# Kernel tuning notes

Measured on AMD Instinct MI355X. Metric: run time of the kernel, lower is better.

## Reference

```python
import jax, jax.numpy as jnp
import numpy as np

B, N, D, H, P = 4, 512, 256, 8, 3
HD = D // H
EPS = 1e-5

def _ln(x, g, b):
    m = jnp.mean(x, axis=-1, keepdims=True)
    v = jnp.var(x, axis=-1, keepdims=True)
    return (x - m) * jax.lax.rsqrt(v + EPS) * g + b

def setup_inputs() -> dict:
    key = jax.random.key(0)
    ks = jax.random.split(key, 12)
    s = lambda *sh: 1.0 / np.sqrt(sh[0])
    return {
        "x": jax.random.normal(ks[0], (B, N, D), jnp.float32),
        "mask": jax.random.randint(ks[1], (B, N), 0, 2).astype(bool),
        "pair_feat": jax.random.normal(ks[2], (B, N, N, P), jnp.float32),
        "Wqkv": jax.random.normal(ks[3], (D, 3 * D), jnp.float32) * s(D),
        "Wout": jax.random.normal(ks[4], (D, D), jnp.float32) * s(D),
        "bout": jnp.zeros((D,), jnp.float32),
        "Wp1": jax.random.normal(ks[5], (P, D), jnp.float32) * s(P),
        "bp1": jnp.zeros((D,), jnp.float32),
        "Wp2": jax.random.normal(ks[6], (D, H), jnp.float32) * s(D),
        "bp2": jnp.zeros((H,), jnp.float32),
        "Wf1": jax.random.normal(ks[7], (D, 4 * D), jnp.float32) * s(D),
        "bf1": jnp.zeros((4 * D,), jnp.float32),
        "Wf2": jax.random.normal(ks[8], (4 * D, D), jnp.float32) * s(4 * D),
        "bf2": jnp.zeros((D,), jnp.float32),
        "g1": jnp.ones((D,), jnp.float32), "b1": jnp.zeros((D,), jnp.float32),
        "g2": jnp.ones((D,), jnp.float32), "b2": jnp.zeros((D,), jnp.float32),
    }

def reference(x, mask, pair_feat, Wqkv, Wout, bout, Wp1, bp1, Wp2, bp2,
              Wf1, bf1, Wf2, bf2, g1, b1, g2, b2):
    b_, n_, d_ = x.shape
    scale = HD ** -0.5
    qkv = x @ Wqkv                                  # [B,N,3D]
    q, k, v = jnp.split(qkv, 3, axis=-1)
    q = q.reshape(b_, n_, H, HD)
    k = k.reshape(b_, n_, H, HD)
    v = v.reshape(b_, n_, H, HD)
    logits = jnp.einsum('bihd,bjhd->bhij', q, k) * scale
    # pairwise bias MLP -> per-head bias [B,H,N,N]
    bias = jax.nn.relu(pair_feat @ Wp1 + bp1) @ Wp2 + bp2   # [B,N,N,H]
    logits = logits + jnp.transpose(bias, (0, 3, 1, 2))
    key_mask = ~mask[:, None, None, :]               # [B,1,1,N]
    logits = jnp.where(key_mask, -1e9, logits)
    attn = jax.nn.softmax(logits, axis=-1)
    out = jnp.einsum('bhij,bjhd->bihd', attn, v).reshape(b_, n_, d_)
    out = out @ Wout + bout
    x = _ln(x + out, g1, b1)
    h = jax.nn.gelu(x @ Wf1 + bf1, approximate=False) @ Wf2 + bf2
    return _ln(x + h, g2, b2)
```

## Files before the change

### kernel.cpp

```cpp
#include <hip/hip_runtime.h>
#include <hip/hip_fp16.h>
#include <math.h>

typedef unsigned short u16;
typedef short s16x8 __attribute__((ext_vector_type(8)));
typedef _Float16 f16x8 __attribute__((ext_vector_type(8)));
typedef float f32x4 __attribute__((ext_vector_type(4)));
typedef unsigned int u32x2 __attribute__((ext_vector_type(2)));

constexpr int CB = 4, CN = 512, CD = 256, CH = 8, CHD = 32;
constexpr float CEPS = 1e-5f;
constexpr int M_ROWS = CB * CN;
constexpr float QSCALE = 0.17677669529663687f;

constexpr size_t O_XB    = 0;
constexpr size_t O_QB    = 1048576;
constexpr size_t O_KB    = 2097152;
constexpr size_t O_VT    = 3145728;
constexpr size_t O_WQKVT = 4194304;
constexpr size_t O_WOUTT = O_WQKVT + 393216;
constexpr size_t O_WF1T  = O_WOUTT + 131072;
constexpr size_t O_WF2T  = O_WF1T + 524288;
constexpr size_t O_WP2T  = O_WF2T + 524288;
constexpr size_t O_PACKED= O_WP2T + 8192;
constexpr size_t O_JIDX  = O_PACKED + 4096;
constexpr size_t O_BIAS  = O_JIDX + 8192;
constexpr size_t O_AOUT  = O_BIAS + 16777216;
constexpr size_t O_H1B   = O_AOUT + 1048576;
constexpr size_t O_PRE1  = O_H1B + 4194304;
constexpr size_t O_PRE2  = O_PRE1 + 2097152;
constexpr size_t O_CNT   = O_PRE2 + 2097152;
constexpr size_t O_IPOS  = O_CNT + 256;

__device__ inline u16 f2b(float f) {
  union { float f; unsigned u; } v{f};
  return (u16)((v.u + 0x7FFFu + ((v.u >> 16) & 1u)) >> 16);
}
__device__ inline float b2f(u16 b) {
  union { unsigned u; float f; } v{(unsigned)b << 16};
  return v.f;
}
__device__ inline f32x4 MFMA(s16x8 a, s16x8 b, f32x4 c) {
  return __builtin_amdgcn_mfma_f32_16x16x32_bf16(a, b, c, 0, 0, 0);
}
__device__ inline f32x4 MFMAH(f16x8 a, f16x8 b, f32x4 c) {
  return __builtin_amdgcn_mfma_f32_16x16x32_f16(a, b, c, 0, 0, 0);
}
__device__ inline unsigned cvtpk(float lo, float hi) {
  unsigned r;
  asm("v_cvt_pk_bf16_f32 %0, %1, %2" : "=v"(r) : "v"(lo), "v"(hi));
  return r;
}
__device__ inline unsigned pkmax0(unsigned a) {
  unsigned d;
  asm("v_pk_max_f16 %0, %1, 0" : "=v"(d) : "v"(a));
  return d;
}

__global__ __launch_bounds__(256) void prep_kernel(
    const float* __restrict__ x, const float* __restrict__ Wqkv,
    const float* __restrict__ Wp2,
    const float* __restrict__ Wp1, const float* __restrict__ bp1,
    const unsigned char* __restrict__ maskraw,
    u16* __restrict__ xb, u16* __restrict__ wqkvt, u16* __restrict__ wp2t,
    unsigned* __restrict__ packed, int* __restrict__ jidxg,
    int* __restrict__ cntg, int* __restrict__ iposg) {
  __shared__ int mode_max;
  __shared__ int mdec[2048];
  int blk = blockIdx.x, tid = threadIdx.x;
  if (blk < 256) {
    for (int t = tid; t < 512; t += 256) {
      float4 v = ((const float4*)x)[blk * 512 + t];
      u16 o0 = f2b(v.x), o1 = f2b(v.y), o2 = f2b(v.z), o3 = f2b(v.w);
      u32x2 w; w.x = (unsigned)o0 | ((unsigned)o1 << 16);
      w.y = (unsigned)o2 | ((unsigned)o3 << 16);
      *(u32x2*)(xb + (size_t)(blk * 512 + t) * 4) = w;
    }
  } else if (blk < 352) {
    int o0 = (blk - 256) * 2048;
    for (int t = tid; t < 2048; t += 256) {
      int o = o0 + t, n = o >> 8, k = o & 255;
      wqkvt[o] = f2b(Wqkv[k * 768 + n]);
    }
  } else if (blk == 352) {
    for (int t = tid; t < 4096; t += 256) {
      int h = t >> 8, c = t & 255;
      wp2t[t] = (h < 8) ? __half_as_ushort(__float2half(Wp2[c * 8 + h])) : (u16)0;
    }
    if (tid < 128) {
      int p = tid * 2;
      unsigned w0 = (unsigned)__half_as_ushort(__float2half(Wp1[p]))
                  | ((unsigned)__half_as_ushort(__float2half(Wp1[p + 1])) << 16);
      unsigned w1 = (unsigned)__half_as_ushort(__float2half(Wp1[256 + p]))
                  | ((unsigned)__half_as_ushort(__float2half(Wp1[256 + p + 1])) << 16);
      unsigned w2 = (unsigned)__half_as_ushort(__float2half(Wp1[512 + p]))
                  | ((unsigned)__half_as_ushort(__float2half(Wp1[512 + p + 1])) << 16);
      unsigned bb = (unsigned)__half_as_ushort(__float2half(bp1[p]))
                  | ((unsigned)__half_as_ushort(__float2half(bp1[p + 1])) << 16);
      uint4 o; o.x = w0; o.y = w1; o.z = w2; o.w = bb;
      ((uint4*)packed)[tid] = o;
    }
  } else {
    if (tid == 0) mode_max = 0;
    __syncthreads();
    int lm = 0;
    for (int i = tid; i < CB*CN; i += 256)
      if ((i & 3) != 0) lm = max(lm, (int)maskraw[i]);
    atomicMax(&mode_max, lm);
    __syncthreads();
    int mv = mode_max;
    for (int i = tid; i < CB*CN; i += 256) {
      int val;
      if (mv == 0)      val = (((const int*)maskraw)[i] != 0);
      else if (mv == 1) val = (maskraw[i] != 0);
      else              val = (((const unsigned int*)maskraw)[i] != 0);
      mdec[i] = val;
    }
    __syncthreads();
    int w = tid >> 6, lane = tid & 63;
    if (w < 4) {
      int b = w, basei = 0, basem = 0;
      for (int c = 0; c < 8; ++c) {
        int j = c * 64 + lane;
        int m = mdec[b * 512 + j];
        unsigned long long bal = __ballot(m != 0);
        int off  = __popcll(bal & ((1ull << lane) - 1ull));
        int offm = __popcll(~bal & ((1ull << lane) - 1ull));
        int pos;
        if (m) { pos = basei + off; jidxg[b * 512 + pos] = j; }
        else   { pos = 511 - (basem + offm); }
        iposg[b * 512 + j] = pos;
        basei += (int)__popcll(bal);
        basem += (int)(64 - __popcll(bal));
      }
      if (lane == 0) cntg[b] = basei;
      for (int p = basei + lane; p < 512; p += 64) jidxg[b * 512 + p] = 0;
    }
  }
}

__global__ __launch_bounds__(256) void qkv_pbias_kernel(
    const u16* __restrict__ A, const u16* __restrict__ Wt,
    u16* __restrict__ qb, u16* __restrict__ kb, u16* __restrict__ vt,
    const float* __restrict__ pf, const unsigned* __restrict__ packed,
    const u16* __restrict__ wp2t, const float* __restrict__ bp2,
    const int* __restrict__ jidxg, const int* __restrict__ cntg,
    const int* __restrict__ iposg, u16* __restrict__ biasc,
    const float* __restrict__ Wout, const float* __restrict__ Wf1,
    const float* __restrict__ Wf2, u16* __restrict__ woutt,
    u16* __restrict__ wf1t, u16* __restrict__ wf2t) {
  __shared__ uint4 smem[1024];
  const int blk = blockIdx.x, tid = threadIdx.x;
  const int lane = tid & 63, w = tid >> 6;
  if (blk < 384) {
    u16* As = (u16*)smem;
    u16* Bs = (u16*)smem + 64 * 64;
    const int wm = w >> 1, wn = w & 1;
    const int bm = (blk / 12) * 64, bn = (blk % 12) * 64;
    f32x4 fz = {0.f, 0.f, 0.f, 0.f};
    f32x4 acc[2][2] = {{fz, fz}, {fz, fz}};
    for (int k0 = 0; k0 < 256; k0 += 64) {
#pragma unroll
      for (int t = tid; t < 512; t += 256) {
        int r = t >> 3, s = t & 7;
        s16x8 v = *(const s16x8*)(A + (size_t)(bm + r) * 256 + k0 + s * 8);
        *(s16x8*)(As + r * 64 + ((s ^ (r & 7)) << 3)) = v;
      }
#pragma unroll
      for (int t = tid; t < 512; t += 256) {
        int r = t >> 3, s = t & 7;
        s16x8 v = *(const s16x8*)(Wt + (size_t)(bn + r) * 256 + k0 + s * 8);
        *(s16x8*)(Bs + r * 64 + ((s ^ (r & 7)) << 3)) = v;
      }
      __syncthreads();
#pragma unroll
      for (int ks = 0; ks < 2; ++ks) {
        s16x8 af[2], bf[2];
#pragma unroll
        for (int mf = 0; mf < 2; ++mf) {
          int r = wm * 32 + mf * 16 + (lane & 15);
          int s = ks * 4 + (lane >> 4);
          af[mf] = *(const s16x8*)(As + r * 64 + ((s ^ (r & 7)) << 3));
        }
#pragma unroll
        for (int nf = 0; nf < 2; ++nf) {
          int r = wn * 32 + nf * 16 + (lane & 15);
          int s = ks * 4 + (lane >> 4);
          bf[nf] = *(const s16x8*)(Bs + r * 64 + ((s ^ (r & 7)) << 3));
        }
#pragma unroll
        for (int mf = 0; mf < 2; ++mf)
#pragma unroll
          for (int nf = 0; nf < 2; ++nf)
            acc[mf][nf] = MFMA(af[mf], bf[nf], acc[mf][nf]);
      }
      __syncthreads();
    }
#pragma unroll
    for (int mf = 0; mf < 2; ++mf) {
#pragma unroll
      for (int nf = 0; nf < 2; ++nf) {
#pragma unroll
        for (int r = 0; r < 4; ++r) {
          int m = bm + wm * 32 + mf * 16 + (lane >> 4) * 4 + r;
          int n = bn + wn * 32 + nf * 16 + (lane & 15);
          float v = acc[mf][nf][r];
          if (n < 256) {
            qb[(size_t)m * 256 + n] = f2b(v * QSCALE);
          } else if (n < 512) {
            kb[(size_t)m * 256 + (n - 256)] = f2b(v);
          } else {
            int nv = n - 512, h = nv >> 5, d = nv & 31;
            int bb = m >> 9, j = m & 511;
            int pos = iposg[bb * 512 + j];
            vt[(size_t)((bb * 8 + h) * 32 + d) * 512 + pos] = f2b(v);
          }
        }
      }
    }
  } else if (blk < 2432) {
    uint4* pk = smem;
    float* pfl = (float*)(smem + 128);
    int* ji = (int*)(smem + 512);
    const int bid = blk - 384;
    const int b = bid >> 9, i = bid & 511;
    const int q = lane >> 4, hr = lane & 15;
    if (tid < 128) pk[tid] = ((const uint4*)packed)[tid];
    const float4* pfr = (const float4*)(pf + (size_t)(b * 512 + i) * 1536);
#pragma unroll
    for (int t = tid; t < 384; t += 256) ((float4*)pfl)[t] = pfr[t];
    for (int t = tid; t < 512; t += 256) ji[t] = jidxg[b * 512 + t];
    const int cnt = cntg[b];
    __syncthreads();
    __half2 f0d[8], f1d[8], f2d[8];
#pragma unroll
    for (int t = 0; t < 8; ++t) {
      int g = t * 4 + w;
      if (g * 16 < cnt) {
        int jsrc = ji[g * 16 + hr];
        f0d[t] = __float2half2_rn(pfl[jsrc * 3 + 0]);
        f1d[t] = __float2half2_rn(pfl[jsrc * 3 + 1]);
        f2d[t] = __float2half2_rn(pfl[jsrc * 3 + 2]);
      }
    }
    f32x4 fz = {0.f, 0.f, 0.f, 0.f};
    f32x4 acc[8] = {fz, fz, fz, fz, fz, fz, fz, fz};
    for (int chunk = 0; chunk < 8; ++chunk) {
      f16x8 wfrag = *(const f16x8*)(wp2t + hr * 256 + chunk * 32 + q * 8);
      int pbase = chunk * 16 + q * 4;
      __half2 w0[4], w1[4], w2[4], bb[4];
#pragma unroll
      for (int p = 0; p < 4; ++p) {
        uint4 c = pk[pbase + p];
        w0[p] = *(const __half2*)&c.x;
        w1[p] = *(const __half2*)&c.y;
        w2[p] = *(const __half2*)&c.z;
        bb[p] = *(const __half2*)&c.w;
      }
#pragma unroll
      for (int t = 0; t < 8; ++t) {
        int g = t * 4 + w;
        if (g * 16 < cnt) {
          union { unsigned u[4]; f16x8 v; } af;
#pragma unroll
          for (int p = 0; p < 4; ++p) {
            __half2 h = __hfma2(f0d[t], w0[p], bb[p]);
            h = __hfma2(f1d[t], w1[p], h);
            h = __hfma2(f2d[t], w2[p], h);
            af.u[p] = pkmax0(*(const unsigned*)&h);
          }
          acc[t] = MFMAH(af.v, wfrag, acc[t]);
        }
      }
    }
    if (hr < 8) {
      float bb = bp2[hr];
      size_t base = ((size_t)(b * 8 + hr) * 512 + i) * 512;
#pragma unroll
      for (int t = 0; t < 8; ++t) {
        int g = t * 4 + w;
        if (g * 16 < cnt) {
          int p0 = g * 16 + q * 4;
          u32x2 o;
          o.x = cvtpk(acc[t][0] + bb, acc[t][1] + bb);
          o.y = cvtpk(acc[t][2] + bb, acc[t][3] + bb);
          *(u32x2*)(biasc + base + p0) = o;
        }
      }
    }
  } else if (blk < 2464) {
    int o0 = (blk - 2432) * 2048;
    for (int t = tid; t < 2048; t += 256) {
      int o = o0 + t, n = o >> 8, k = o & 255;
      woutt[o] = f2b(Wout[k * 256 + n]);
    }
  } else if (blk < 2592) {
    int o0 = (blk - 2464) * 2048;
    for (int t = tid; t < 2048; t += 256) {
      int o = o0 + t, n = o >> 8, k = o & 255;
      wf1t[o] = f2b(Wf1[k * 1024 + n]);
    }
  } else {
    int o0 = (blk - 2592) * 2048;
    for (int t = tid; t < 2048; t += 256) {
      int o = o0 + t, n = o >> 10, k = o & 1023;
      wf2t[o] = f2b(Wf2[k * 256 + n]);
    }
  }
}

__global__ __launch_bounds__(512) void flash_kernel(
    const u16* __restrict__ qb, const u16* __restrict__ kb,
    const u16* __restrict__ vt, const u16* __restrict__ biasc,
    const int* __restrict__ jidxg, const int* __restrict__ cntg,
    u16* __restrict__ aout) {
  const int i0 = blockIdx.x * 64, h = blockIdx.y, b = blockIdx.z;
  const int tid = threadIdx.x;
  const int lane = tid & 63, w = tid >> 6;
  const int mf = w & 3, jhalf = w >> 2;
  __shared__ u16 qs[64 * 32];
  __shared__ u16 ksh[128 * 32];
  __shared__ u16 vs[32 * 128];
  __shared__ u16 ps[8][16 * 64];
  __shared__ float cmb[4][2][16][2];
  __shared__ int ji[512];
  for (int t = tid; t < 512; t += 512) ji[t] = jidxg[b * 512 + t];
  for (int t = tid; t < 256; t += 512) {
    int r = t >> 2, s = t & 3;
    s16x8 v = *(const s16x8*)(qb + (size_t)(b * 512 + i0 + r) * 256 + h * 32 + s * 8);
    *(s16x8*)(qs + r * 32 + ((s ^ (r & 3)) << 3)) = v;
  }
  const int cnt = cntg[b];
  __syncthreads();
  f32x4 fz = {0.f, 0.f, 0.f, 0.f};
  f32x4 oacc[2] = {fz, fz};
  float mrun[4] = {-3e38f, -3e38f, -3e38f, -3e38f};
  float lrun[4] = {0.f, 0.f, 0.f, 0.f};
  const int jj0 = jhalf * 64;
  const int il = mf * 16 + (lane >> 4) * 4;
  const u16* bbase = biasc + ((size_t)((b * 8 + h) * 512 + i0 + il)) * 512
                   + jj0 + (lane & 15);
  const int NJT = (cnt + 127) >> 7;
  for (int jc = 0; jc < NJT; ++jc) {
    int j0 = jc * 128;
    {
      int r = tid >> 2, s = tid & 3;
      int jsrc = ji[j0 + r];
      s16x8 v = *(const s16x8*)(kb + (size_t)(b * 512 + jsrc) * 256 + h * 32 + s * 8);
      *(s16x8*)(ksh + r * 32 + ((s ^ (r & 3)) << 3)) = v;
    }
    {
      int r = tid >> 4, s = tid & 15;
      s16x8 v = *(const s16x8*)(vt + (size_t)((b * 8 + h) * 32 + r) * 512 + j0 + s * 8);
      *(s16x8*)(vs + r * 128 + (((s & 8) | ((s & 7) ^ (r & 7))) << 3)) = v;
    }
    u16 bvr[4][4];
#pragma unroll
    for (int jf = 0; jf < 4; ++jf)
#pragma unroll
      for (int r = 0; r < 4; ++r)
        bvr[jf][r] = bbase[(size_t)r * 512 + j0 + jf * 16];
    __syncthreads();
    int mk[4];
#pragma unroll
    for (int jf = 0; jf < 4; ++jf)
      mk[jf] = (j0 + jj0 + jf * 16 + (lane & 15)) < cnt;
    int arow = mf * 16 + (lane & 15);
    s16x8 af = *(const s16x8*)(qs + arow * 32 + (((lane >> 4) ^ (arow & 3)) << 3));
    f32x4 sm[4];
#pragma unroll
    for (int jf = 0; jf < 4; ++jf) {
      int brow = jj0 + jf * 16 + (lane & 15);
      s16x8 bfr = *(const s16x8*)(ksh + brow * 32 + (((lane >> 4) ^ (brow & 3)) << 3));
      sm[jf] = MFMA(af, bfr, fz);
    }
#pragma unroll
    for (int jf = 0; jf < 4; ++jf) {
#pragma unroll
      for (int r = 0; r < 4; ++r) {
        float sval = sm[jf][r] + b2f(bvr[jf][r]);
        sm[jf][r] = mk[jf] ? sval : -1e9f;
      }
    }
    float mx[4];
#pragma unroll
    for (int r = 0; r < 4; ++r)
      mx[r] = fmaxf(fmaxf(sm[0][r], sm[1][r]), fmaxf(sm[2][r], sm[3][r]));
#pragma unroll
    for (int d = 1; d < 16; d <<= 1)
#pragma unroll
      for (int r = 0; r < 4; ++r) mx[r] = fmaxf(mx[r], __shfl_xor(mx[r], d));
    float psl[4] = {0.f, 0.f, 0.f, 0.f};
#pragma unroll
    for (int jf = 0; jf < 4; ++jf)
#pragma unroll
      for (int r = 0; r < 4; ++r) {
        float p = __expf(sm[jf][r] - mx[r]);
        sm[jf][r] = p; psl[r] += p;
      }
#pragma unroll
    for (int d = 1; d < 16; d <<= 1)
#pragma unroll
      for (int r = 0; r < 4; ++r) psl[r] += __shfl_xor(psl[r], d);
    if ((lane & 15) == 0) {
#pragma unroll
      for (int r = 0; r < 4; ++r) {
        int row = (lane >> 4) * 4 + r;
        cmb[mf][jhalf][row][0] = mx[r];
        cmb[mf][jhalf][row][1] = psl[r];
      }
    }
    __syncthreads();
    float selfs[4];
#pragma unroll
    for (int r = 0; r < 4; ++r) {
      int row = (lane >> 4) * 4 + r;
      float omx = cmb[mf][1 - jhalf][row][0];
      float ops = cmb[mf][1 - jhalf][row][1];
      float tm = fmaxf(mx[r], omx);
      float nm = fmaxf(mrun[r], tm);
      float sc = __expf(mrun[r] - nm);
      selfs[r] = __expf(mx[r] - nm);
      float ptile = psl[r] * selfs[r] + ops * __expf(omx - nm);
      lrun[r] = lrun[r] * sc + ptile;
      mrun[r] = nm;
      oacc[0][r] *= sc; oacc[1][r] *= sc;
    }
    u16* pw = &ps[w][0];
#pragma unroll
    for (int jf = 0; jf < 4; ++jf) {
      int jcol = jf * 16 + (lane & 15);
      int slot = jcol >> 3, el = jcol & 7;
#pragma unroll
      for (int r = 0; r < 4; ++r) {
        int row = (lane >> 4) * 4 + r;
        pw[row * 64 + ((slot ^ (row & 7)) << 3) + el] = f2b(sm[jf][r] * selfs[r]);
      }
    }
#pragma unroll
    for (int kw = 0; kw < 2; ++kw) {
      int prow = lane & 15;
      s16x8 pa = *(const s16x8*)(pw + prow * 64 + (((kw * 4 + (lane >> 4)) ^ (prow & 7)) << 3));
#pragma unroll
      for (int df = 0; df < 2; ++df) {
        int drow = df * 16 + (lane & 15);
        int jcol = jj0 + kw * 32 + ((lane >> 4) << 3);
        int slot = jcol >> 3;
        s16x8 vv = *(const s16x8*)(vs + drow * 128 + (((slot & 8) | ((slot & 7) ^ (drow & 7))) << 3));
        oacc[df] = MFMA(pa, vv, oacc[df]);
      }
    }
    __syncthreads();
  }
  float* obuf = (float*)&ps[0][0];
  if (jhalf == 1) {
#pragma unroll
    for (int r = 0; r < 4; ++r) {
      int row = mf * 16 + (lane >> 4) * 4 + r;
#pragma unroll
      for (int df = 0; df < 2; ++df)
        obuf[row * 33 + df * 16 + (lane & 15)] = oacc[df][r];
    }
  }
  __syncthreads();
  if (jhalf == 0) {
#pragma unroll
    for (int r = 0; r < 4; ++r) {
      float inv = 1.0f / lrun[r];
      int row = mf * 16 + (lane >> 4) * 4 + r;
      int i = i0 + row;
#pragma unroll
      for (int df = 0; df < 2; ++df) {
        int d = df * 16 + (lane & 15);
        float o = (oacc[df][r] + obuf[row * 33 + d]) * inv;
        aout[(size_t)(b * 512 + i) * 256 + h * 32 + d] = f2b(o);
      }
    }
  }
}

__global__ __launch_bounds__(256) void mgemm_res(
    const u16* __restrict__ A, const u16* __restrict__ Wt,
    const float* __restrict__ bias, const float* __restrict__ R,
    float* __restrict__ outf, int N, int K) {
  __shared__ u16 As[32 * 64];
  __shared__ u16 Bs[64 * 64];
  const int tid = threadIdx.x;
  const int lane = tid & 63, w = tid >> 6;
  const int wm = w >> 1, wn = w & 1;
  const int bm = blockIdx.y * 32, bn = blockIdx.x * 64;
  f32x4 fz = {0.f, 0.f, 0.f, 0.f};
  f32x4 acc[2] = {fz, fz};
  for (int k0 = 0; k0 < K; k0 += 64) {
    for (int t = tid; t < 256; t += 256) {
      int r = t >> 3, s = t & 7;
      s16x8 v = *(const s16x8*)(A + (size_t)(bm + r) * K + k0 + s * 8);
      *(s16x8*)(As + r * 64 + ((s ^ (r & 7)) << 3)) = v;
    }
#pragma unroll
    for (int t = tid; t < 512; t += 256) {
      int r = t >> 3, s = t & 7;
      s16x8 v = *(const s16x8*)(Wt + (size_t)(bn + r) * K + k0 + s * 8);
      *(s16x8*)(Bs + r * 64 + ((s ^ (r & 7)) << 3)) = v;
    }
    __syncthreads();
#pragma unroll
    for (int ks = 0; ks < 2; ++ks) {
      int r = wm * 16 + (lane & 15);
      int s = ks * 4 + (lane >> 4);
      s16x8 af = *(const s16x8*)(As + r * 64 + ((s ^ (r & 7)) << 3));
#pragma unroll
      for (int nf = 0; nf < 2; ++nf) {
        int br = wn * 32 + nf * 16 + (lane & 15);
        s16x8 bf = *(const s16x8*)(Bs + br * 64 + ((s ^ (br & 7)) << 3));
        acc[nf] = MFMA(af, bf, acc[nf]);
      }
    }
    __syncthreads();
  }
#pragma unroll
  for (int nf = 0; nf < 2; ++nf) {
#pragma unroll
    for (int r = 0; r < 4; ++r) {
      int m = bm + wm * 16 + (lane >> 4) * 4 + r;
      int n = bn + wn * 32 + nf * 16 + (lane & 15);
      outf[(size_t)m * N + n] = acc[nf][r] + bias[n] + R[(size_t)m * N + n];
    }
  }
}

__global__ __launch_bounds__(256) void ffn1_kernel(
    const float* __restrict__ pre1, const u16* __restrict__ Wt,
    const float* __restrict__ bias, const float* __restrict__ g1,
    const float* __restrict__ b1, u16* __restrict__ outb) {
  __shared__ u16 As[64 * 64];
  __shared__ u16 Bs[64 * 64];
  __shared__ float rowm[64], rowr[64];
  const int tid = threadIdx.x;
  const int lane = tid & 63, w = tid >> 6;
  const int wm = w >> 1, wn = w & 1;
  const int bm = blockIdx.y * 64, bn = blockIdx.x * 64;
  {
    int r = tid >> 2, qd = tid & 3;
    const float4* pr = (const float4*)(pre1 + (size_t)(bm + r) * 256 + qd * 64);
    float s = 0.f, ss = 0.f;
#pragma unroll
    for (int u = 0; u < 16; ++u) {
      float4 v = pr[u];
      s += v.x + v.y + v.z + v.w;
      ss += v.x*v.x + v.y*v.y + v.z*v.z + v.w*v.w;
    }
    s += __shfl_xor(s, 1); ss += __shfl_xor(ss, 1);
    s += __shfl_xor(s, 2); ss += __shfl_xor(ss, 2);
    if (qd == 0) {
      float mean = s * (1.0f / 256.0f);
      float var  = ss * (1.0f / 256.0f) - mean * mean;
      rowm[r] = mean; rowr[r] = rsqrtf(var + CEPS);
    }
  }
  __syncthreads();
  f32x4 fz = {0.f, 0.f, 0.f, 0.f};
  f32x4 acc[2][2] = {{fz, fz}, {fz, fz}};
  for (int k0 = 0; k0 < 256; k0 += 64) {
#pragma unroll
    for (int t = tid; t < 512; t += 256) {
      int r = t >> 3, s = t & 7;
      float mean = rowm[r], rstd = rowr[r];
      const float4* pr = (const float4*)(pre1 + (size_t)(bm + r) * 256 + k0 + s * 8);
      float4 a0 = pr[0], a1 = pr[1];
      const float4* gp = (const float4*)(g1 + k0 + s * 8);
      const float4* bp = (const float4*)(b1 + k0 + s * 8);
      float4 g0 = gp[0], g1v = gp[1], c0 = bp[0], c1 = bp[1];
      union { unsigned u[4]; s16x8 v; } pk2;
      pk2.u[0] = cvtpk((a0.x-mean)*rstd*g0.x + c0.x, (a0.y-mean)*rstd*g0.y + c0.y);
      pk2.u[1] = cvtpk((a0.z-mean)*rstd*g0.z + c0.z, (a0.w-mean)*rstd*g0.w + c0.w);
      pk2.u[2] = cvtpk((a1.x-mean)*rstd*g1v.x + c1.x, (a1.y-mean)*rstd*g1v.y + c1.y);
      pk2.u[3] = cvtpk((a1.z-mean)*rstd*g1v.z + c1.z, (a1.w-mean)*rstd*g1v.w + c1.w);
      *(s16x8*)(As + r * 64 + ((s ^ (r & 7)) << 3)) = pk2.v;
    }
#pragma unroll
    for (int t = tid; t < 512; t += 256) {
      int r = t >> 3, s = t & 7;
      s16x8 v = *(const s16x8*)(Wt + (size_t)(bn + r) * 256 + k0 + s * 8);
      *(s16x8*)(Bs + r * 64 + ((s ^ (r & 7)) << 3)) = v;
    }
    __syncthreads();
#pragma unroll
    for (int ks = 0; ks < 2; ++ks) {
      s16x8 af[2], bf[2];
#pragma unroll
      for (int mf = 0; mf < 2; ++mf) {
        int r = wm * 32 + mf * 16 + (lane & 15);
        int s = ks * 4 + (lane >> 4);
        af[mf] = *(const s16x8*)(As + r * 64 + ((s ^ (r & 7)) << 3));
      }
#pragma unroll
      for (int nf = 0; nf < 2; ++nf) {
        int r = wn * 32 + nf * 16 + (lane & 15);
        int s = ks * 4 + (lane >> 4);
        bf[nf] = *(const s16x8*)(Bs + r * 64 + ((s ^ (r & 7)) << 3));
      }
#pragma unroll
      for (int mf = 0; mf < 2; ++mf)
#pragma unroll
        for (int nf = 0; nf < 2; ++nf)
          acc[mf][nf] = MFMA(af[mf], bf[nf], acc[mf][nf]);
    }
    __syncthreads();
  }
#pragma unroll
  for (int mf = 0; mf < 2; ++mf) {
#pragma unroll
    for (int nf = 0; nf < 2; ++nf) {
#pragma unroll
      for (int r = 0; r < 4; ++r) {
        int m = bm + wm * 32 + mf * 16 + (lane >> 4) * 4 + r;
        int n = bn + wn * 32 + nf * 16 + (lane & 15);
        float gv = acc[mf][nf][r] + bias[n];
        gv = 0.5f * gv * (1.0f + erff(gv * 0.70710678118654752f));
        outb[(size_t)m * 1024 + n] = f2b(gv);
      }
    }
  }
}

__global__ __launch_bounds__(256) void ffn2_kernel(
    const u16* __restrict__ A, const u16* __restrict__ Wt,
    const float* __restrict__ bias, const float* __restrict__ pre1,
    const float* __restrict__ g1, const float* __restrict__ b1,
    float* __restrict__ outf) {
  __shared__ u16 As[32 * 64];
  __shared__ u16 Bs[64 * 64];
  __shared__ float rowm[32], rowr[32];
  const int tid = threadIdx.x;
  const int lane = tid & 63, w = tid >> 6;
  const int wm = w >> 1, wn = w & 1;
  const int bm = blockIdx.y * 32, bn = blockIdx.x * 64;
  {
    int r = tid >> 3, od = tid & 7;
    const float4* pr = (const float4*)(pre1 + (size_t)(bm + r) * 256 + od * 32);
    float s = 0.f, ss = 0.f;
#pragma unroll
    for (int u = 0; u < 8; ++u) {
      float4 v = pr[u];
      s += v.x + v.y + v.z + v.w;
      ss += v.x*v.x + v.y*v.y + v.z*v.z + v.w*v.w;
    }
    s += __shfl_xor(s, 1); ss += __shfl_xor(ss, 1);
    s += __shfl_xor(s, 2); ss += __shfl_xor(ss, 2);
    s += __shfl_xor(s, 4); ss += __shfl_xor(ss, 4);
    if (od == 0) {
      float mean = s * (1.0f / 256.0f);
      float var  = ss * (1.0f / 256.0f) - mean * mean;
      rowm[r] = mean; rowr[r] = rsqrtf(var + CEPS);
    }
  }
  __syncthreads();
  f32x4 fz = {0.f, 0.f, 0.f, 0.f};
  f32x4 acc[2] = {fz, fz};
  for (int k0 = 0; k0 < 1024; k0 += 64) {
    for (int t = tid; t < 256; t += 256) {
      int r = t >> 3, s = t & 7;
      s16x8 v = *(const s16x8*)(A + (size_t)(bm + r) * 1024 + k0 + s * 8);
      *(s16x8*)(As + r * 64 + ((s ^ (r & 7)) << 3)) = v;
    }
#pragma unroll
    for (int t = tid; t < 512; t += 256) {
      int r = t >> 3, s = t & 7;
      s16x8 v = *(const s16x8*)(Wt + (size_t)(bn + r) * 1024 + k0 + s * 8);
      *(s16x8*)(Bs + r * 64 + ((s ^ (r & 7)) << 3)) = v;
    }
    __syncthreads();
#pragma unroll
    for (int ks = 0; ks < 2; ++ks) {
      int r = wm * 16 + (lane & 15);
      int s = ks * 4 + (lane >> 4);
      s16x8 af = *(const s16x8*)(As + r * 64 + ((s ^ (r & 7)) << 3));
#pragma unroll
      for (int nf = 0; nf < 2; ++nf) {
        int br = wn * 32 + nf * 16 + (lane & 15);
        s16x8 bf = *(const s16x8*)(Bs + br * 64 + ((s ^ (br & 7)) << 3));
        acc[nf] = MFMA(af, bf, acc[nf]);
      }
    }
    __syncthreads();
  }
#pragma unroll
  for (int nf = 0; nf < 2; ++nf) {
#pragma unroll
    for (int r = 0; r < 4; ++r) {
      int m = bm + wm * 16 + (lane >> 4) * 4 + r;
      int n = bn + wn * 32 + nf * 16 + (lane & 15);
      float mean = rowm[m - bm], rstd = rowr[m - bm];
      float xr = (pre1[(size_t)m * 256 + n] - mean) * rstd * g1[n] + b1[n];
      outf[(size_t)m * 256 + n] = acc[nf][r] + bias[n] + xr;
    }
  }
}

__global__ __launch_bounds__(256) void ln_kernel(
    const float* __restrict__ in, const float* __restrict__ g,
    const float* __restrict__ be, float* __restrict__ op) {
  int row = blockIdx.x * 4 + (threadIdx.x >> 6);
  int lane = threadIdx.x & 63;
  const float* x = in + (size_t)row * CD;
  float4 v = *(const float4*)&x[lane * 4];
  float s  = v.x + v.y + v.z + v.w;
  float ss = v.x*v.x + v.y*v.y + v.z*v.z + v.w*v.w;
#pragma unroll
  for (int off = 32; off > 0; off >>= 1) {
    s  += __shfl_xor(s, off);
    ss += __shfl_xor(ss, off);
  }
  float mean = s * (1.0f / CD);
  float var  = ss * (1.0f / CD) - mean * mean;
  float inv  = rsqrtf(var + CEPS);
  float4 gg = *(const float4*)&g[lane * 4];
  float4 bb = *(const float4*)&be[lane * 4];
  float4 o;
  o.x = (v.x - mean) * inv * gg.x + bb.x;
  o.y = (v.y - mean) * inv * gg.y + bb.y;
  o.z = (v.z - mean) * inv * gg.z + bb.z;
  o.w = (v.w - mean) * inv * gg.w + bb.w;
  *(float4*)&op[(size_t)row * CD + lane * 4] = o;
}

extern "C" void kernel_launch(void* const* d_in, const int* in_sizes, int n_in,
                              void* d_out, int out_size, void* d_ws, size_t ws_size,
                              hipStream_t stream) {
  (void)in_sizes; (void)n_in; (void)out_size; (void)ws_size;
  const float* x    = (const float*)d_in[0];
  const void*  mask = d_in[1];
  const float* pf   = (const float*)d_in[2];
  const float* Wqkv = (const float*)d_in[3];
  const float* Wout = (const float*)d_in[4];
  const float* bout = (const float*)d_in[5];
  const float* Wp1  = (const float*)d_in[6];
  const float* bp1  = (const float*)d_in[7];
  const float* Wp2  = (const float*)d_in[8];
  const float* bp2  = (const float*)d_in[9];
  const float* Wf1  = (const float*)d_in[10];
  const float* bf1  = (const float*)d_in[11];
  const float* Wf2  = (const float*)d_in[12];
  const float* bf2  = (const float*)d_in[13];
  const float* g1   = (const float*)d_in[14];
  const float* b1   = (const float*)d_in[15];
  const float* g2   = (const float*)d_in[16];
  const float* b2   = (const float*)d_in[17];

  char* ws = (char*)d_ws;
  u16* xb     = (u16*)(ws + O_XB);
  u16* qb     = (u16*)(ws + O_QB);
  u16* kb     = (u16*)(ws + O_KB);
  u16* vt     = (u16*)(ws + O_VT);
  u16* wqkvt  = (u16*)(ws + O_WQKVT);
  u16* woutt  = (u16*)(ws + O_WOUTT);
  u16* wf1t   = (u16*)(ws + O_WF1T);
  u16* wf2t   = (u16*)(ws + O_WF2T);
  u16* wp2t   = (u16*)(ws + O_WP2T);
  unsigned* packed = (unsigned*)(ws + O_PACKED);
  int* jidxg  = (int*)(ws + O_JIDX);
  int* cntg   = (int*)(ws + O_CNT);
  int* iposg  = (int*)(ws + O_IPOS);
  u16* biasc  = (u16*)(ws + O_BIAS);
  u16* aout   = (u16*)(ws + O_AOUT);
  u16* h1b    = (u16*)(ws + O_H1B);
  float* pre1 = (float*)(ws + O_PRE1);
  float* pre2 = (float*)(ws + O_PRE2);
  float* out  = (float*)d_out;

  hipLaunchKernelGGL(prep_kernel, dim3(354), dim3(256), 0, stream,
                     x, Wqkv, Wp2, Wp1, bp1,
                     (const unsigned char*)mask,
                     xb, wqkvt, wp2t, packed, jidxg, cntg, iposg);
  hipLaunchKernelGGL(qkv_pbias_kernel, dim3(2720), dim3(256), 0, stream,
                     xb, wqkvt, qb, kb, vt,
                     pf, packed, wp2t, bp2, jidxg, cntg, iposg, biasc,
                     Wout, Wf1, Wf2, woutt, wf1t, wf2t);
  hipLaunchKernelGGL(flash_kernel, dim3(8, 8, 4), dim3(512), 0, stream,
                     qb, kb, vt, biasc, jidxg, cntg, aout);
  hipLaunchKernelGGL(mgemm_res, dim3(4, 64), dim3(256), 0, stream,
                     aout, woutt, bout, x, pre1, 256, 256);
  hipLaunchKernelGGL(ffn1_kernel, dim3(16, 32), dim3(256), 0, stream,
                     pre1, wf1t, bf1, g1, b1, h1b);
  hipLaunchKernelGGL(ffn2_kernel, dim3(4, 64), dim3(256), 0, stream,
                     h1b, wf2t, bf2, pre1, g1, b1, pre2);
  hipLaunchKernelGGL(ln_kernel, dim3(M_ROWS / 4), dim3(256), 0, stream,
                     pre2, g2, b2, out);
}
```

Before: 95.37 us.

## Fuse layernorms into full-row output GEMM epilogues and drop standalone LN kernel

```diff
diff --git a/kernel.cpp b/kernel.cpp
--- a/kernel.cpp
+++ b/kernel.cpp
@@ -27,9 +27,9 @@
 constexpr size_t O_BIAS  = O_JIDX + 8192;
 constexpr size_t O_AOUT  = O_BIAS + 16777216;
 constexpr size_t O_H1B   = O_AOUT + 1048576;
-constexpr size_t O_PRE1  = O_H1B + 4194304;
-constexpr size_t O_PRE2  = O_PRE1 + 2097152;
-constexpr size_t O_CNT   = O_PRE2 + 2097152;
+constexpr size_t O_X1B   = O_H1B + 4194304;
+constexpr size_t O_XRF   = O_X1B + 1048576;
+constexpr size_t O_CNT   = O_XRF + 2097152;
 constexpr size_t O_IPOS  = O_CNT + 256;
 
 __device__ inline u16 f2b(float f) {
@@ -479,104 +479,113 @@
   }
 }
 
-__global__ __launch_bounds__(256) void mgemm_res(
+__global__ __launch_bounds__(256) void gemm_ln1_kernel(
     const u16* __restrict__ A, const u16* __restrict__ Wt,
-    const float* __restrict__ bias, const float* __restrict__ R,
-    float* __restrict__ outf, int N, int K) {
-  __shared__ u16 As[32 * 64];
+    const float* __restrict__ bias, const float* __restrict__ x,
+    const float* __restrict__ g1, const float* __restrict__ b1,
+    u16* __restrict__ x1b, float* __restrict__ xrf) {
+  __shared__ u16 As[16 * 64];
+  __shared__ u16 Bs[256 * 64];
+  __shared__ float part[16][4][2];
+  __shared__ float rowm[16], rowr[16];
+  const int tid = threadIdx.x;
+  const int lane = tid & 63, w = tid >> 6;
+  const int bm = blockIdx.x * 16;
+  f32x4 fz = {0.f, 0.f, 0.f, 0.f};
+  f32x4 acc[4] = {fz, fz, fz, fz};
+  for (int k0 = 0; k0 < 256; k0 += 64) {
+    if (tid < 128) {
+      int r = tid >> 3, s = tid & 7;
+      s16x8 v = *(const s16x8*)(A + (size_t)(bm + r) * 256 + k0 + s * 8);
+      *(s16x8*)(As + r * 64 + ((s ^ (r & 7)) << 3)) = v;
+    }
+#pragma unroll
+    for (int t = tid; t < 2048; t += 256) {
+      int r = t >> 3, s = t & 7;
+      s16x8 v = *(const s16x8*)(Wt + (size_t)r * 256 + k0 + s * 8);
+      *(s16x8*)(Bs + r * 64 + ((s ^ (r & 7)) << 3)) = v;
+    }
+    __syncthreads();
+#pragma unroll
+    for (int ks = 0; ks < 2; ++ks) {
+      int ar = lane & 15, as = ks * 4 + (lane >> 4);
+      s16x8 af = *(const s16x8*)(As + ar * 64 + ((as ^ (ar & 7)) << 3));
+#pragma unroll
+      for (int nf = 0; nf < 4; ++nf) {
+        int br = w * 64 + nf * 16 + (lane & 15);
+        s16x8 bf = *(const s16x8*)(Bs + br * 64 + ((as ^ (br & 7)) << 3));
+        acc[nf] = MFMA(af, bf, acc[nf]);
+      }
+    }
+    __syncthreads();
+  }
+  float v[4][4];
+  float sp[4] = {0.f, 0.f, 0.f, 0.f}, ssp[4] = {0.f, 0.f, 0.f, 0.f};
+#pragma unroll
+  for (int nf = 0; nf < 4; ++nf) {
+    int col = w * 64 + nf * 16 + (lane & 15);
+#pragma unroll
+    for (int r = 0; r < 4; ++r) {
+      int row = (lane >> 4) * 4 + r;
+      float val = acc[nf][r] + bias[col] + x[(size_t)(bm + row) * 256 + col];
+      v[nf][r] = val;
+      sp[r] += val; ssp[r] += val * val;
+    }
+  }
+#pragma unroll
+  for (int d = 1; d < 16; d <<= 1)
+#pragma unroll
+    for (int r = 0; r < 4; ++r) {
+      sp[r]  += __shfl_xor(sp[r], d);
+      ssp[r] += __shfl_xor(ssp[r], d);
+    }
+  if ((lane & 15) == 0) {
+#pragma unroll
+    for (int r = 0; r < 4; ++r) {
+      int row = (lane >> 4) * 4 + r;
+      part[row][w][0] = sp[r];
+      part[row][w][1] = ssp[r];
+    }
+  }
+  __syncthreads();
+  if (tid < 16) {
+    float s = part[tid][0][0] + part[tid][1][0] + part[tid][2][0] + part[tid][3][0];
+    float ss = part[tid][0][1] + part[tid][1][1] + part[tid][2][1] + part[tid][3][1];
+    float mean = s * (1.0f / 256.0f);
+    float var  = ss * (1.0f / 256.0f) - mean * mean;
+    rowm[tid] = mean; rowr[tid] = rsqrtf(var + CEPS);
+  }
+  __syncthreads();
+#pragma unroll
+  for (int nf = 0; nf < 4; ++nf) {
+    int col = w * 64 + nf * 16 + (lane & 15);
+#pragma unroll
+    for (int r = 0; r < 4; ++r) {
+      int row = (lane >> 4) * 4 + r;
+      float xr = (v[nf][r] - rowm[row]) * rowr[row] * g1[col] + b1[col];
+      xrf[(size_t)(bm + row) * 256 + col] = xr;
+      x1b[(size_t)(bm + row) * 256 + col] = f2b(xr);
+    }
+  }
+}
+
+__global__ __launch_bounds__(256) void ffn1_kernel(
+    const u16* __restrict__ A, const u16* __restrict__ Wt,
+    const float* __restrict__ bias, u16* __restrict__ outb) {
+  __shared__ u16 As[64 * 64];
   __shared__ u16 Bs[64 * 64];
   const int tid = threadIdx.x;
   const int lane = tid & 63, w = tid >> 6;
   const int wm = w >> 1, wn = w & 1;
-  const int bm = blockIdx.y * 32, bn = blockIdx.x * 64;
-  f32x4 fz = {0.f, 0.f, 0.f, 0.f};
-  f32x4 acc[2] = {fz, fz};
-  for (int k0 = 0; k0 < K; k0 += 64) {
-    for (int t = tid; t < 256; t += 256) {
-      int r = t >> 3, s = t & 7;
-      s16x8 v = *(const s16x8*)(A + (size_t)(bm + r) * K + k0 + s * 8);
-      *(s16x8*)(As + r * 64 + ((s ^ (r & 7)) << 3)) = v;
-    }
-#pragma unroll
-    for (int t = tid; t < 512; t += 256) {
-      int r = t >> 3, s = t & 7;
-      s16x8 v = *(const s16x8*)(Wt + (size_t)(bn + r) * K + k0 + s * 8);
-      *(s16x8*)(Bs + r * 64 + ((s ^ (r & 7)) << 3)) = v;
-    }
-    __syncthreads();
-#pragma unroll
-    for (int ks = 0; ks < 2; ++ks) {
-      int r = wm * 16 + (lane & 15);
-      int s = ks * 4 + (lane >> 4);
-      s16x8 af = *(const s16x8*)(As + r * 64 + ((s ^ (r & 7)) << 3));
-#pragma unroll
-      for (int nf = 0; nf < 2; ++nf) {
-        int br = wn * 32 + nf * 16 + (lane & 15);
-        s16x8 bf = *(const s16x8*)(Bs + br * 64 + ((s ^ (br & 7)) << 3));
-        acc[nf] = MFMA(af, bf, acc[nf]);
-      }
-    }
-    __syncthreads();
-  }
-#pragma unroll
-  for (int nf = 0; nf < 2; ++nf) {
-#pragma unroll
-    for (int r = 0; r < 4; ++r) {
-      int m = bm + wm * 16 + (lane >> 4) * 4 + r;
-      int n = bn + wn * 32 + nf * 16 + (lane & 15);
-      outf[(size_t)m * N + n] = acc[nf][r] + bias[n] + R[(size_t)m * N + n];
-    }
-  }
-}
-
-__global__ __launch_bounds__(256) void ffn1_kernel(
-    const float* __restrict__ pre1, const u16* __restrict__ Wt,
-    const float* __restrict__ bias, const float* __restrict__ g1,
-    const float* __restrict__ b1, u16* __restrict__ outb) {
-  __shared__ u16 As[64 * 64];
-  __shared__ u16 Bs[64 * 64];
-  __shared__ float rowm[64], rowr[64];
-  const int tid = threadIdx.x;
-  const int lane = tid & 63, w = tid >> 6;
-  const int wm = w >> 1, wn = w & 1;
   const int bm = blockIdx.y * 64, bn = blockIdx.x * 64;
-  {
-    int r = tid >> 2, qd = tid & 3;
-    const float4* pr = (const float4*)(pre1 + (size_t)(bm + r) * 256 + qd * 64);
-    float s = 0.f, ss = 0.f;
-#pragma unroll
-    for (int u = 0; u < 16; ++u) {
-      float4 v = pr[u];
-      s += v.x + v.y + v.z + v.w;
-      ss += v.x*v.x + v.y*v.y + v.z*v.z + v.w*v.w;
-    }
-    s += __shfl_xor(s, 1); ss += __shfl_xor(ss, 1);
-    s += __shfl_xor(s, 2); ss += __shfl_xor(ss, 2);
-    if (qd == 0) {
-      float mean = s * (1.0f / 256.0f);
-      float var  = ss * (1.0f / 256.0f) - mean * mean;
-      rowm[r] = mean; rowr[r] = rsqrtf(var + CEPS);
-    }
-  }
-  __syncthreads();
   f32x4 fz = {0.f, 0.f, 0.f, 0.f};
   f32x4 acc[2][2] = {{fz, fz}, {fz, fz}};
   for (int k0 = 0; k0 < 256; k0 += 64) {
 #pragma unroll
     for (int t = tid; t < 512; t += 256) {
       int r = t >> 3, s = t & 7;
-      float mean = rowm[r], rstd = rowr[r];
-      const float4* pr = (const float4*)(pre1 + (size_t)(bm + r) * 256 + k0 + s * 8);
-      float4 a0 = pr[0], a1 = pr[1];
-      const float4* gp = (const float4*)(g1 + k0 + s * 8);
-      const float4* bp = (const float4*)(b1 + k0 + s * 8);
-      float4 g0 = gp[0], g1v = gp[1], c0 = bp[0], c1 = bp[1];
-      union { unsigned u[4]; s16x8 v; } pk2;
-      pk2.u[0] = cvtpk((a0.x-mean)*rstd*g0.x + c0.x, (a0.y-mean)*rstd*g0.y + c0.y);
-      pk2.u[1] = cvtpk((a0.z-mean)*rstd*g0.z + c0.z, (a0.w-mean)*rstd*g0.w + c0.w);
-      pk2.u[2] = cvtpk((a1.x-mean)*rstd*g1v.x + c1.x, (a1.y-mean)*rstd*g1v.y + c1.y);
-      pk2.u[3] = cvtpk((a1.z-mean)*rstd*g1v.z + c1.z, (a1.w-mean)*rstd*g1v.w + c1.w);
-      *(s16x8*)(As + r * 64 + ((s ^ (r & 7)) << 3)) = pk2.v;
+      s16x8 v = *(const s16x8*)(A + (size_t)(bm + r) * 256 + k0 + s * 8);
+      *(s16x8*)(As + r * 64 + ((s ^ (r & 7)) << 3)) = v;
     }
 #pragma unroll
     for (int t = tid; t < 512; t += 256) {
@@ -624,105 +633,93 @@
   }
 }
 
-__global__ __launch_bounds__(256) void ffn2_kernel(
+__global__ __launch_bounds__(256) void gemm_ln2_kernel(
     const u16* __restrict__ A, const u16* __restrict__ Wt,
-    const float* __restrict__ bias, const float* __restrict__ pre1,
-    const float* __restrict__ g1, const float* __restrict__ b1,
-    float* __restrict__ outf) {
-  __shared__ u16 As[32 * 64];
-  __shared__ u16 Bs[64 * 64];
-  __shared__ float rowm[32], rowr[32];
+    const float* __restrict__ bias, const float* __restrict__ xrf,
+    const float* __restrict__ g2, const float* __restrict__ b2,
+    float* __restrict__ out) {
+  __shared__ u16 As[16 * 64];
+  __shared__ u16 Bs[256 * 64];
+  __shared__ float part[16][4][2];
+  __shared__ float rowm[16], rowr[16];
   const int tid = threadIdx.x;
   const int lane = tid & 63, w = tid >> 6;
-  const int wm = w >> 1, wn = w & 1;
-  const int bm = blockIdx.y * 32, bn = blockIdx.x * 64;
-  {
-    int r = tid >> 3, od = tid & 7;
-    const float4* pr = (const float4*)(pre1 + (size_t)(bm + r) * 256 + od * 32);
-    float s = 0.f, ss = 0.f;
-#pragma unroll
-    for (int u = 0; u < 8; ++u) {
-      float4 v = pr[u];
-      s += v.x + v.y + v.z + v.w;
-      ss += v.x*v.x + v.y*v.y + v.z*v.z + v.w*v.w;
-    }
-    s += __shfl_xor(s, 1); ss += __shfl_xor(ss, 1);
-    s += __shfl_xor(s, 2); ss += __shfl_xor(ss, 2);
-    s += __shfl_xor(s, 4); ss += __shfl_xor(ss, 4);
-    if (od == 0) {
-      float mean = s * (1.0f / 256.0f);
-      float var  = ss * (1.0f / 256.0f) - mean * mean;
-      rowm[r] = mean; rowr[r] = rsqrtf(var + CEPS);
-    }
-  }
-  __syncthreads();
+  const int bm = blockIdx.x * 16;
   f32x4 fz = {0.f, 0.f, 0.f, 0.f};
-  f32x4 acc[2] = {fz, fz};
+  f32x4 acc[4] = {fz, fz, fz, fz};
   for (int k0 = 0; k0 < 1024; k0 += 64) {
-    for (int t = tid; t < 256; t += 256) {
-      int r = t >> 3, s = t & 7;
+    if (tid < 128) {
+      int r = tid >> 3, s = tid & 7;
       s16x8 v = *(const s16x8*)(A + (size_t)(bm + r) * 1024 + k0 + s * 8);
       *(s16x8*)(As + r * 64 + ((s ^ (r & 7)) << 3)) = v;
     }
 #pragma unroll
-    for (int t = tid; t < 512; t += 256) {
+    for (int t = tid; t < 2048; t += 256) {
       int r = t >> 3, s = t & 7;
-      s16x8 v = *(const s16x8*)(Wt + (size_t)(bn + r) * 1024 + k0 + s * 8);
+      s16x8 v = *(const s16x8*)(Wt + (size_t)r * 1024 + k0 + s * 8);
       *(s16x8*)(Bs + r * 64 + ((s ^ (r & 7)) << 3)) = v;
     }
     __syncthreads();
 #pragma unroll
     for (int ks = 0; ks < 2; ++ks) {
-      int r = wm * 16 + (lane & 15);
-      int s = ks * 4 + (lane >> 4);
-      s16x8 af = *(const s16x8*)(As + r * 64 + ((s ^ (r & 7)) << 3));
-#pragma unroll
-      for (int nf = 0; nf < 2; ++nf) {
-        int br = wn * 32 + nf * 16 + (lane & 15);
-        s16x8 bf = *(const s16x8*)(Bs + br * 64 + ((s ^ (br & 7)) << 3));
+      int ar = lane & 15, as = ks * 4 + (lane >> 4);
+      s16x8 af = *(const s16x8*)(As + ar * 64 + ((as ^ (ar & 7)) << 3));
+#pragma unroll
+      for (int nf = 0; nf < 4; ++nf) {
+        int br = w * 64 + nf * 16 + (lane & 15);
+        s16x8 bf = *(const s16x8*)(Bs + br * 64 + ((as ^ (br & 7)) << 3));
         acc[nf] = MFMA(af, bf, acc[nf]);
       }
     }
     __syncthreads();
   }
-#pragma unroll
-  for (int nf = 0; nf < 2; ++nf) {
-#pragma unroll
-    for (int r = 0; r < 4; ++r) {
-      int m = bm + wm * 16 + (lane >> 4) * 4 + r;
-      int n = bn + wn * 32 + nf * 16 + (lane & 15);
-      float mean = rowm[m - bm], rstd = rowr[m - bm];
-      float xr = (pre1[(size_t)m * 256 + n] - mean) * rstd * g1[n] + b1[n];
-      outf[(size_t)m * 256 + n] = acc[nf][r] + bias[n] + xr;
-    }
-  }
-}
-
-__global__ __launch_bounds__(256) void ln_kernel(
-    const float* __restrict__ in, const float* __restrict__ g,
-    const float* __restrict__ be, float* __restrict__ op) {
-  int row = blockIdx.x * 4 + (threadIdx.x >> 6);
-  int lane = threadIdx.x & 63;
-  const float* x = in + (size_t)row * CD;
-  float4 v = *(const float4*)&x[lane * 4];
-  float s  = v.x + v.y + v.z + v.w;
-  float ss = v.x*v.x + v.y*v.y + v.z*v.z + v.w*v.w;
-#pragma unroll
-  for (int off = 32; off > 0; off >>= 1) {
-    s  += __shfl_xor(s, off);
-    ss += __shfl_xor(ss, off);
-  }
-  float mean = s * (1.0f / CD);
-  float var  = ss * (1.0f / CD) - mean * mean;
-  float inv  = rsqrtf(var + CEPS);
-  float4 gg = *(const float4*)&g[lane * 4];
-  float4 bb = *(const float4*)&be[lane * 4];
-  float4 o;
-  o.x = (v.x - mean) * inv * gg.x + bb.x;
-  o.y = (v.y - mean) * inv * gg.y + bb.y;
-  o.z = (v.z - mean) * inv * gg.z + bb.z;
-  o.w = (v.w - mean) * inv * gg.w + bb.w;
-  *(float4*)&op[(size_t)row * CD + lane * 4] = o;
+  float v[4][4];
+  float sp[4] = {0.f, 0.f, 0.f, 0.f}, ssp[4] = {0.f, 0.f, 0.f, 0.f};
+#pragma unroll
+  for (int nf = 0; nf < 4; ++nf) {
+    int col = w * 64 + nf * 16 + (lane & 15);
+#pragma unroll
+    for (int r = 0; r < 4; ++r) {
+      int row = (lane >> 4) * 4 + r;
+      float val = acc[nf][r] + bias[col] + xrf[(size_t)(bm + row) * 256 + col];
+      v[nf][r] = val;
+      sp[r] += val; ssp[r] += val * val;
+    }
+  }
+#pragma unroll
+  for (int d = 1; d < 16; d <<= 1)
+#pragma unroll
+    for (int r = 0; r < 4; ++r) {
+      sp[r]  += __shfl_xor(sp[r], d);
+      ssp[r] += __shfl_xor(ssp[r], d);
+    }
+  if ((lane & 15) == 0) {
+#pragma unroll
+    for (int r = 0; r < 4; ++r) {
+      int row = (lane >> 4) * 4 + r;
+      part[row][w][0] = sp[r];
+      part[row][w][1] = ssp[r];
+    }
+  }
+  __syncthreads();
+  if (tid < 16) {
+    float s = part[tid][0][0] + part[tid][1][0] + part[tid][2][0] + part[tid][3][0];
+    float ss = part[tid][0][1] + part[tid][1][1] + part[tid][2][1] + part[tid][3][1];
+    float mean = s * (1.0f / 256.0f);
+    float var  = ss * (1.0f / 256.0f) - mean * mean;
+    rowm[tid] = mean; rowr[tid] = rsqrtf(var + CEPS);
+  }
+  __syncthreads();
+#pragma unroll
+  for (int nf = 0; nf < 4; ++nf) {
+    int col = w * 64 + nf * 16 + (lane & 15);
+#pragma unroll
+    for (int r = 0; r < 4; ++r) {
+      int row = (lane >> 4) * 4 + r;
+      out[(size_t)(bm + row) * 256 + col] =
+          (v[nf][r] - rowm[row]) * rowr[row] * g2[col] + b2[col];
+    }
+  }
 }
 
 extern "C" void kernel_launch(void* const* d_in, const int* in_sizes, int n_in,
@@ -765,8 +762,8 @@
   u16* biasc  = (u16*)(ws + O_BIAS);
   u16* aout   = (u16*)(ws + O_AOUT);
   u16* h1b    = (u16*)(ws + O_H1B);
-  float* pre1 = (float*)(ws + O_PRE1);
-  float* pre2 = (float*)(ws + O_PRE2);
+  u16* x1b    = (u16*)(ws + O_X1B);
+  float* xrf  = (float*)(ws + O_XRF);
   float* out  = (float*)d_out;
 
   hipLaunchKernelGGL(prep_kernel, dim3(354), dim3(256), 0, stream,
@@ -779,12 +776,10 @@
                      Wout, Wf1, Wf2, woutt, wf1t, wf2t);
   hipLaunchKernelGGL(flash_kernel, dim3(8, 8, 4), dim3(512), 0, stream,
                      qb, kb, vt, biasc, jidxg, cntg, aout);
-  hipLaunchKernelGGL(mgemm_res, dim3(4, 64), dim3(256), 0, stream,
-                     aout, woutt, bout, x, pre1, 256, 256);
+  hipLaunchKernelGGL(gemm_ln1_kernel, dim3(128), dim3(256), 0, stream,
+                     aout, woutt, bout, x, g1, b1, x1b, xrf);
   hipLaunchKernelGGL(ffn1_kernel, dim3(16, 32), dim3(256), 0, stream,
-                     pre1, wf1t, bf1, g1, b1, h1b);
-  hipLaunchKernelGGL(ffn2_kernel, dim3(4, 64), dim3(256), 0, stream,
-                     h1b, wf2t, bf2, pre1, g1, b1, pre2);
-  hipLaunchKernelGGL(ln_kernel, dim3(M_ROWS / 4), dim3(256), 0, stream,
-                     pre2, g2, b2, out);
-}
+                     x1b, wf1t, bf1, h1b);
+  hipLaunchKernelGGL(gemm_ln2_kernel, dim3(128), dim3(256), 0, stream,
+                     h1b, wf2t, bf2, xrf, g2, b2, out);
+}
```

New measurement: 104.1 us. +9.2%, slower.
